# Kernel optimization log

Measured on AMD Instinct MI355X. Metric: run time of the kernel, lower is better.

## Reference

```python
import jax, jax.numpy as jnp
import numpy as np

B = 64                      # batch_size
MAX_STEPS = 100
FEAT = 6 + MAX_STEPS        # 106
REPEATS = 10
D = REPEATS * FEAT          # 1060
H = 256                     # policy_hidden_size
COUNTS = 32 * np.arange(B) + 16   # ragged segment sizes, sum=65536, max=2032
N = int(COUNTS.sum())
MAXLEN = int(COUNTS.max())
BN_EPS = 1e-5
LRELU_SLOPE = 0.01


def setup_inputs() -> dict:
    key = jax.random.key(0)
    k = jax.random.split(key, 6)
    seg = np.repeat(np.arange(B), COUNTS).astype(np.float32)  # column 0 = batch index
    features = jax.random.normal(k[0], (N, 1 + FEAT), jnp.float32)
    features = features.at[:, 0].set(jnp.asarray(seg))
    W1 = jax.random.normal(k[1], (D, H), jnp.float32) / np.sqrt(D)
    b1 = jax.random.normal(k[2], (H,), jnp.float32) * 0.01
    W2 = jax.random.normal(k[3], (H, 1), jnp.float32) / np.sqrt(H)
    b2 = jax.random.normal(k[4], (1,), jnp.float32) * 0.01
    return {
        "features": features,
        "bn_gamma": jnp.ones((D,), jnp.float32),
        "bn_beta": jnp.zeros((D,), jnp.float32),
        "W1": W1, "b1": b1, "W2": W2, "b2": b2,
        "max_len": MAXLEN,
    }


def reference(features, bn_gamma, bn_beta, W1, b1, W2, b2, max_len):
    seg = features[:, 0].astype(jnp.int32)                 # [N] batch indices
    x = jnp.tile(features[:, 1:], (1, REPEATS))            # [N, D] repeated features
    # BatchNorm1d (training mode: biased batch stats, as in the torch default)
    mean = jnp.mean(x, axis=0)
    var = jnp.var(x, axis=0)
    xn = (x - mean) * jax.lax.rsqrt(var + BN_EPS) * bn_gamma + bn_beta
    h = jnp.dot(xn, W1) + b1                               # [N, H]
    h = jnp.where(h >= 0, h, LRELU_SLOPE * h)              # LeakyReLU
    logits = (jnp.dot(h, W2) + b2)[:, 0]                   # [N]
    # segmented (ragged) log_softmax over each batch element's nodes
    m = jax.ops.segment_max(logits, seg, num_segments=B)   # [B]
    z = logits - m[seg]
    s = jax.ops.segment_sum(jnp.exp(z), seg, num_segments=B)
    logp = z - jnp.log(s)[seg]                             # [N]
    # scatter into padded [B, max_len] (-inf padding), position = rank within segment
    cnts = jax.ops.segment_sum(jnp.ones_like(seg), seg, num_segments=B)
    starts = jnp.cumsum(cnts) - cnts                       # exclusive prefix sum
    pos = jnp.arange(N, dtype=jnp.int32) - starts[seg]
    out = jnp.full((B, max_len), -jnp.inf, jnp.float32)
    return out.at[seg, pos].set(logp)
```

## Files before the change

kernel.cpp:

```cpp
#include <hip/hip_runtime.h>
#include <math.h>

#define NROWS   65536
#define NFEAT   106
#define NCOLIN  107
#define DREP    10
#define HID     256
#define BATCH   64
#define MAXLEN  2032
#define BN_EPS  1e-5f
#define SLOPE   0.01f
#define KPAD    128
#define NB_STATS 512
#define NEG_BIG (-1.0e30f)

#define WS_PART   0
#define WS_BACC   (WS_PART + NB_STATS*212)
#define WS_W1T    (WS_BACC + HID)
#define WS_FT     (WS_W1T + (HID*KPAD)/2)
#define WS_LOGITS (WS_FT + (NROWS*KPAD)/2)

typedef __attribute__((ext_vector_type(8))) short short8v;
typedef __attribute__((ext_vector_type(4))) float f32x4;

__device__ inline unsigned short f2bf(float x) {
    unsigned int u = __float_as_uint(x);
    return (unsigned short)((u + 0x7FFFu + ((u >> 16) & 1u)) >> 16);
}

__device__ __forceinline__ void gload_lds16(const void* g, void* l) {
    __builtin_amdgcn_global_load_lds(
        (const __attribute__((address_space(1))) void*)(g),
        (__attribute__((address_space(3))) void*)(l), 16, 0, 0);
}

__global__ __launch_bounds__(256) void k_stats(const float* __restrict__ feat,
                                               const float* __restrict__ b1,
                                               float* __restrict__ ws) {
    int tid  = threadIdx.x;
    int wave = tid >> 6, lane = tid & 63;
    int gw   = blockIdx.x * 4 + wave;
    if (blockIdx.x == 0) ws[WS_BACC + tid] = b1[tid];

    unsigned char* ft = (unsigned char*)(ws + WS_FT);
    int c0 = 2 * lane, c1 = 2 * lane + 1;
    bool act = (lane < 53);
    float s0 = 0.f, q0 = 0.f, s1 = 0.f, q1 = 0.f;
    for (int r = gw; r < NROWS; r += 2048) {
        const float* row = feat + (size_t)r * NCOLIN + 1;
        float v0 = 0.f, v1 = 0.f;
        if (act) { v0 = row[c0]; v1 = row[c1]; }
        s0 += v0; q0 += v0 * v0;
        s1 += v1; q1 += v1 * v1;
        unsigned int u = ((unsigned int)f2bf(v1) << 16) | f2bf(v0);
        *(unsigned int*)(ft + (size_t)r * 256 + lane * 4) = u;
    }
    __shared__ float red[4][64][4];
    red[wave][lane][0] = s0; red[wave][lane][1] = q0;
    red[wave][lane][2] = s1; red[wave][lane][3] = q1;
    __syncthreads();
    if (tid < 53) {
        float S0 = 0.f, Q0 = 0.f, S1 = 0.f, Q1 = 0.f;
        for (int w = 0; w < 4; ++w) {
            S0 += red[w][tid][0]; Q0 += red[w][tid][1];
            S1 += red[w][tid][2]; Q1 += red[w][tid][3];
        }
        float* p = ws + WS_PART + blockIdx.x * 212;
        p[2 * tid] = S0; p[2 * tid + 1] = S1;
        p[106 + 2 * tid] = Q0; p[107 + 2 * tid] = Q1;
    }
}

__global__ __launch_bounds__(256) void k_fold2(const float* __restrict__ gamma,
                                               const float* __restrict__ beta,
                                               const float* __restrict__ W1,
                                               float* __restrict__ ws) {
    int k = blockIdx.x;
    int j = threadIdx.x;
    unsigned char* w1t = (unsigned char*)(ws + WS_W1T);
    int byteW = j * 256 + ((2 * k) ^ ((j & 7) << 4));
    if (k >= NFEAT) { *(unsigned short*)(w1t + byteW) = 0; return; }

    float S = ws[WS_PART + j * 212 + k]       + ws[WS_PART + (j + 256) * 212 + k];
    float Q = ws[WS_PART + j * 212 + 106 + k] + ws[WS_PART + (j + 256) * 212 + 106 + k];
    #pragma unroll
    for (int o = 32; o > 0; o >>= 1) { S += __shfl_xor(S, o); Q += __shfl_xor(Q, o); }
    __shared__ float r8[8];
    int w = j >> 6, l = j & 63;
    if (l == 0) { r8[w * 2] = S; r8[w * 2 + 1] = Q; }
    __syncthreads();
    S = r8[0] + r8[2] + r8[4] + r8[6];
    Q = r8[1] + r8[3] + r8[5] + r8[7];

    float mean = S * (1.0f / NROWS);
    float var  = Q * (1.0f / NROWS) - mean * mean;
    float rstd = rsqrtf(var + BN_EPS);

    float accW = 0.f, accB = 0.f;
    #pragma unroll
    for (int r = 0; r < DREP; ++r) {
        int d = r * NFEAT + k;
        float wv = W1[(size_t)d * HID + j];
        accW += gamma[d] * wv;
        accB += beta[d]  * wv;
    }
    float a = accW * rstd;
    *(unsigned short*)(w1t + byteW) = f2bf(a);
    atomicAdd(&ws[WS_BACC + j], accB - mean * a);
}

__global__ __launch_bounds__(256) void k_mlp4(const float* __restrict__ W2,
                                              const float* __restrict__ b2,
                                              float* __restrict__ ws) {
    __shared__ __align__(16) unsigned char wl[65536];
    int tid = threadIdx.x;
    int w = tid >> 6, l = tid & 63;
    int lq = l >> 4, ln = l & 15;

    const unsigned char* wsrc = (const unsigned char*)(ws + WS_W1T);
    #pragma unroll
    for (int i = 0; i < 16; ++i)
        gload_lds16(wsrc + (w * 16 + i) * 1024 + l * 16, wl + (w * 16 + i) * 1024);

    int rowBase = blockIdx.x * 128 + w * 32;
    const unsigned char* ab = (const unsigned char*)(ws + WS_FT) + (size_t)rowBase * 256;
    short8v a[2][4];
    #pragma unroll
    for (int t = 0; t < 2; ++t)
        #pragma unroll
        for (int ks = 0; ks < 4; ++ks)
            a[t][ks] = *(const short8v*)(ab + t * 4096 + ln * 256 + ks * 64 + lq * 16);

    float b1r[16], w2r[16];
    #pragma unroll
    for (int ct = 0; ct < 16; ++ct) {
        b1r[ct] = ws[WS_BACC + ct * 16 + ln];
        w2r[ct] = W2[ct * 16 + ln];
    }
    float bias2 = b2[0];
    __syncthreads();

    float sp[2][4] = {{0.f,0.f,0.f,0.f},{0.f,0.f,0.f,0.f}};
    #pragma unroll
    for (int ct = 0; ct < 16; ++ct) {
        int j = ct * 16 + ln;
        int sw = (j & 7) << 4;
        short8v bq[4];
        #pragma unroll
        for (int ks = 0; ks < 4; ++ks)
            bq[ks] = *(const short8v*)(wl + j * 256 + ((ks * 64 + lq * 16) ^ sw));
        #pragma unroll
        for (int t = 0; t < 2; ++t) {
            f32x4 acc = {b1r[ct], b1r[ct], b1r[ct], b1r[ct]};
            #pragma unroll
            for (int ks = 0; ks < 4; ++ks)
                acc = __builtin_amdgcn_mfma_f32_16x16x32_bf16(a[t][ks], bq[ks], acc, 0, 0, 0);
            #pragma unroll
            for (int reg = 0; reg < 4; ++reg) {
                float h = acc[reg];
                h = (h >= 0.f) ? h : SLOPE * h;
                sp[t][reg] += h * w2r[ct];
            }
        }
    }
    #pragma unroll
    for (int t = 0; t < 2; ++t)
        #pragma unroll
        for (int reg = 0; reg < 4; ++reg) {
            float s = sp[t][reg];
            s += __shfl_xor(s, 1); s += __shfl_xor(s, 2);
            s += __shfl_xor(s, 4); s += __shfl_xor(s, 8);
            if (ln == 0)
                ws[WS_LOGITS + rowBase + t * 16 + lq * 4 + reg] = s + bias2;
        }
}

__global__ __launch_bounds__(256) void k_softmax(const float* __restrict__ ws,
                                                 float* __restrict__ out) {
    int b = blockIdx.x;
    int tid = threadIdx.x;
    int cnt = 32 * b + 16;
    int start = 16 * b * b;
    __shared__ float cache[MAXLEN];
    __shared__ float red[8];
    const float* lg = ws + WS_LOGITS + start;
    for (int i = tid; i < cnt; i += 256) cache[i] = lg[i];
    __syncthreads();

    float m = -1.0e30f;
    for (int i = tid; i < cnt; i += 256) m = fmaxf(m, cache[i]);
    #pragma unroll
    for (int o = 32; o > 0; o >>= 1) m = fmaxf(m, __shfl_xor(m, o));
    int wave = tid >> 6, lane = tid & 63;
    if (lane == 0) red[wave] = m;
    __syncthreads();
    m = fmaxf(fmaxf(red[0], red[1]), fmaxf(red[2], red[3]));

    float s = 0.f;
    for (int i = tid; i < cnt; i += 256) s += expf(cache[i] - m);
    #pragma unroll
    for (int o = 32; o > 0; o >>= 1) s += __shfl_xor(s, o);
    if (lane == 0) red[4 + wave] = s;
    __syncthreads();
    s = red[4] + red[5] + red[6] + red[7];
    float logC = m + logf(s);

    float* op = out + (size_t)b * MAXLEN;
    for (int i = tid; i < MAXLEN; i += 256)
        op[i] = (i < cnt) ? cache[i] - logC : NEG_BIG;
}

extern "C" void kernel_launch(void* const* d_in, const int* in_sizes, int n_in,
                              void* d_out, int out_size, void* d_ws, size_t ws_size,
                              hipStream_t stream) {
    const float* feat  = (const float*)d_in[0];
    const float* gamma = (const float*)d_in[1];
    const float* beta  = (const float*)d_in[2];
    const float* W1    = (const float*)d_in[3];
    const float* b1    = (const float*)d_in[4];
    const float* W2    = (const float*)d_in[5];
    const float* b2    = (const float*)d_in[6];
    float* ws  = (float*)d_ws;
    float* out = (float*)d_out;

    hipLaunchKernelGGL(k_stats,   dim3(NB_STATS), dim3(256), 0, stream, feat, b1, ws);
    hipLaunchKernelGGL(k_fold2,   dim3(KPAD),     dim3(256), 0, stream, gamma, beta, W1, ws);
    hipLaunchKernelGGL(k_mlp4,    dim3(512),      dim3(256), 0, stream, W2, b2, ws);
    hipLaunchKernelGGL(k_softmax, dim3(BATCH),    dim3(256), 0, stream, ws, out);
}
```

Before: 40.62 us.

## Fuse MLP logits with segmented softmax in one per-segment kernel

Merges the MLP and softmax kernels so each block computes the logits of one batch segment straight into shared memory and then runs the log-softmax. This removes one launch and the global logits round trip, and adds register prefetch of the next weight tile. The cost is a grid of only 64 blocks with uneven work, so the largest segment sets the time and most compute units sit idle. The stats kernel also switches to contiguous row chunks per wave.

```diff
diff --git a/kernel.cpp b/kernel.cpp
--- a/kernel.cpp
+++ b/kernel.cpp
@@ -18,7 +18,6 @@
 #define WS_BACC   (WS_PART + NB_STATS*212)
 #define WS_W1T    (WS_BACC + HID)
 #define WS_FT     (WS_W1T + (HID*KPAD)/2)
-#define WS_LOGITS (WS_FT + (NROWS*KPAD)/2)
 
 typedef __attribute__((ext_vector_type(8))) short short8v;
 typedef __attribute__((ext_vector_type(4))) float f32x4;
@@ -39,14 +38,16 @@
                                                float* __restrict__ ws) {
     int tid  = threadIdx.x;
     int wave = tid >> 6, lane = tid & 63;
-    int gw   = blockIdx.x * 4 + wave;
     if (blockIdx.x == 0) ws[WS_BACC + tid] = b1[tid];
 
     unsigned char* ft = (unsigned char*)(ws + WS_FT);
-    int c0 = 2 * lane, c1 = 2 * lane + 1;
+    int c0 = 2 * lane, c1 = c0 + 1;
     bool act = (lane < 53);
+    int r0 = blockIdx.x * 128 + wave * 32;
     float s0 = 0.f, q0 = 0.f, s1 = 0.f, q1 = 0.f;
-    for (int r = gw; r < NROWS; r += 2048) {
+    #pragma unroll 4
+    for (int i = 0; i < 32; ++i) {
+        int r = r0 + i;
         const float* row = feat + (size_t)r * NCOLIN + 1;
         float v0 = 0.f, v1 = 0.f;
         if (act) { v0 = row[c0]; v1 = row[c1]; }
@@ -109,27 +110,25 @@
     atomicAdd(&ws[WS_BACC + j], accB - mean * a);
 }
 
-__global__ __launch_bounds__(256) void k_mlp4(const float* __restrict__ W2,
-                                              const float* __restrict__ b2,
-                                              float* __restrict__ ws) {
+__global__ __launch_bounds__(256) void k_mlpsm(const float* __restrict__ W2,
+                                               const float* __restrict__ b2,
+                                               float* __restrict__ ws,
+                                               float* __restrict__ out) {
     __shared__ __align__(16) unsigned char wl[65536];
+    __shared__ float cache[MAXLEN];
+    __shared__ float red[8];
     int tid = threadIdx.x;
     int w = tid >> 6, l = tid & 63;
     int lq = l >> 4, ln = l & 15;
+    int b = blockIdx.x;
+    int cnt = 32 * b + 16;
+    int start = 16 * b * b;
+    int ntiles = cnt >> 4;
 
     const unsigned char* wsrc = (const unsigned char*)(ws + WS_W1T);
     #pragma unroll
     for (int i = 0; i < 16; ++i)
         gload_lds16(wsrc + (w * 16 + i) * 1024 + l * 16, wl + (w * 16 + i) * 1024);
-
-    int rowBase = blockIdx.x * 128 + w * 32;
-    const unsigned char* ab = (const unsigned char*)(ws + WS_FT) + (size_t)rowBase * 256;
-    short8v a[2][4];
-    #pragma unroll
-    for (int t = 0; t < 2; ++t)
-        #pragma unroll
-        for (int ks = 0; ks < 4; ++ks)
-            a[t][ks] = *(const short8v*)(ab + t * 4096 + ln * 256 + ks * 64 + lq * 16);
 
     float b1r[16], w2r[16];
     #pragma unroll
@@ -140,59 +139,70 @@
     float bias2 = b2[0];
     __syncthreads();
 
-    float sp[2][4] = {{0.f,0.f,0.f,0.f},{0.f,0.f,0.f,0.f}};
-    #pragma unroll
-    for (int ct = 0; ct < 16; ++ct) {
-        int j = ct * 16 + ln;
-        int sw = (j & 7) << 4;
-        short8v bq[4];
-        #pragma unroll
-        for (int ks = 0; ks < 4; ++ks)
-            bq[ks] = *(const short8v*)(wl + j * 256 + ((ks * 64 + lq * 16) ^ sw));
-        #pragma unroll
-        for (int t = 0; t < 2; ++t) {
-            f32x4 acc = {b1r[ct], b1r[ct], b1r[ct], b1r[ct]};
+    const unsigned char* ab = (const unsigned char*)(ws + WS_FT) + (size_t)start * 256;
+    int sw = (ln & 7) << 4;
+
+    for (int t0 = 4 * w; t0 < ntiles; t0 += 16) {
+        short8v a[4][4];
+        #pragma unroll
+        for (int u = 0; u < 4; ++u) {
+            int t = t0 + u;
+            int tc = (t < ntiles) ? t : t0;
+            const unsigned char* ap = ab + (size_t)tc * 4096 + ln * 256 + lq * 16;
             #pragma unroll
             for (int ks = 0; ks < 4; ++ks)
-                acc = __builtin_amdgcn_mfma_f32_16x16x32_bf16(a[t][ks], bq[ks], acc, 0, 0, 0);
+                a[u][ks] = *(const short8v*)(ap + ks * 64);
+        }
+        float sp[4][4] = {{0,0,0,0},{0,0,0,0},{0,0,0,0},{0,0,0,0}};
+        short8v bqc[4], bqn[4];
+        #pragma unroll
+        for (int ks = 0; ks < 4; ++ks)
+            bqc[ks] = *(const short8v*)(wl + ln * 256 + ((ks * 64 + lq * 16) ^ sw));
+        #pragma unroll
+        for (int ct = 0; ct < 16; ++ct) {
+            if (ct < 15) {
+                int j = (ct + 1) * 16 + ln;
+                #pragma unroll
+                for (int ks = 0; ks < 4; ++ks)
+                    bqn[ks] = *(const short8v*)(wl + j * 256 + ((ks * 64 + lq * 16) ^ sw));
+            }
             #pragma unroll
-            for (int reg = 0; reg < 4; ++reg) {
-                float h = acc[reg];
-                h = (h >= 0.f) ? h : SLOPE * h;
-                sp[t][reg] += h * w2r[ct];
+            for (int u = 0; u < 4; ++u) {
+                f32x4 acc = {b1r[ct], b1r[ct], b1r[ct], b1r[ct]};
+                #pragma unroll
+                for (int ks = 0; ks < 4; ++ks)
+                    acc = __builtin_amdgcn_mfma_f32_16x16x32_bf16(a[u][ks], bqc[ks], acc, 0, 0, 0);
+                #pragma unroll
+                for (int reg = 0; reg < 4; ++reg) {
+                    float h = acc[reg];
+                    h = (h >= 0.f) ? h : SLOPE * h;
+                    sp[u][reg] += h * w2r[ct];
+                }
             }
-        }
-    }
-    #pragma unroll
-    for (int t = 0; t < 2; ++t)
-        #pragma unroll
-        for (int reg = 0; reg < 4; ++reg) {
-            float s = sp[t][reg];
-            s += __shfl_xor(s, 1); s += __shfl_xor(s, 2);
-            s += __shfl_xor(s, 4); s += __shfl_xor(s, 8);
-            if (ln == 0)
-                ws[WS_LOGITS + rowBase + t * 16 + lq * 4 + reg] = s + bias2;
-        }
-}
-
-__global__ __launch_bounds__(256) void k_softmax(const float* __restrict__ ws,
-                                                 float* __restrict__ out) {
-    int b = blockIdx.x;
-    int tid = threadIdx.x;
-    int cnt = 32 * b + 16;
-    int start = 16 * b * b;
-    __shared__ float cache[MAXLEN];
-    __shared__ float red[8];
-    const float* lg = ws + WS_LOGITS + start;
-    for (int i = tid; i < cnt; i += 256) cache[i] = lg[i];
+            #pragma unroll
+            for (int ks = 0; ks < 4; ++ks) bqc[ks] = bqn[ks];
+        }
+        #pragma unroll
+        for (int u = 0; u < 4; ++u) {
+            int t = t0 + u;
+            if (t < ntiles) {
+                #pragma unroll
+                for (int reg = 0; reg < 4; ++reg) {
+                    float s = sp[u][reg];
+                    s += __shfl_xor(s, 1); s += __shfl_xor(s, 2);
+                    s += __shfl_xor(s, 4); s += __shfl_xor(s, 8);
+                    if (ln == 0) cache[t * 16 + lq * 4 + reg] = s + bias2;
+                }
+            }
+        }
+    }
     __syncthreads();
 
     float m = -1.0e30f;
     for (int i = tid; i < cnt; i += 256) m = fmaxf(m, cache[i]);
     #pragma unroll
     for (int o = 32; o > 0; o >>= 1) m = fmaxf(m, __shfl_xor(m, o));
-    int wave = tid >> 6, lane = tid & 63;
-    if (lane == 0) red[wave] = m;
+    if (l == 0) red[w] = m;
     __syncthreads();
     m = fmaxf(fmaxf(red[0], red[1]), fmaxf(red[2], red[3]));
 
@@ -200,7 +210,7 @@
     for (int i = tid; i < cnt; i += 256) s += expf(cache[i] - m);
     #pragma unroll
     for (int o = 32; o > 0; o >>= 1) s += __shfl_xor(s, o);
-    if (lane == 0) red[4 + wave] = s;
+    if (l == 0) red[4 + w] = s;
     __syncthreads();
     s = red[4] + red[5] + red[6] + red[7];
     float logC = m + logf(s);
@@ -223,8 +233,7 @@
     float* ws  = (float*)d_ws;
     float* out = (float*)d_out;
 
-    hipLaunchKernelGGL(k_stats,   dim3(NB_STATS), dim3(256), 0, stream, feat, b1, ws);
-    hipLaunchKernelGGL(k_fold2,   dim3(KPAD),     dim3(256), 0, stream, gamma, beta, W1, ws);
-    hipLaunchKernelGGL(k_mlp4,    dim3(512),      dim3(256), 0, stream, W2, b2, ws);
-    hipLaunchKernelGGL(k_softmax, dim3(BATCH),    dim3(256), 0, stream, ws, out);
-}
+    hipLaunchKernelGGL(k_stats, dim3(NB_STATS), dim3(256), 0, stream, feat, b1, ws);
+    hipLaunchKernelGGL(k_fold2, dim3(KPAD),     dim3(256), 0, stream, gamma, beta, W1, ws);
+    hipLaunchKernelGGL(k_mlpsm, dim3(BATCH),    dim3(256), 0, stream, W2, b2, ws, out);
+}
```

Result: slower. 129.6 us (+219.0%).

## Fuse segmented softmax into MLP kernel via last-block-done counters

Applied to the files above, without the earlier changes.

Removes the separate softmax launch. Each MLP block atomically adds its row contributions to per-segment counters, and the block that completes a segment runs that segment's log-softmax and writes the padded output row. The stats kernel also switches to contiguous 32-row chunks per wave, and LeakyReLU becomes an fmax. This saves a launch and its dependency gap, but the softmax tail is serialized onto whichever block finishes each segment and relies on threadfence ordering between blocks.

```diff
diff --git a/kernel.cpp b/kernel.cpp
--- a/kernel.cpp
+++ b/kernel.cpp
@@ -19,6 +19,7 @@
 #define WS_W1T    (WS_BACC + HID)
 #define WS_FT     (WS_W1T + (HID*KPAD)/2)
 #define WS_LOGITS (WS_FT + (NROWS*KPAD)/2)
+#define WS_CTR    (WS_LOGITS + NROWS)
 
 typedef __attribute__((ext_vector_type(8))) short short8v;
 typedef __attribute__((ext_vector_type(4))) float f32x4;
@@ -39,14 +40,16 @@
                                                float* __restrict__ ws) {
     int tid  = threadIdx.x;
     int wave = tid >> 6, lane = tid & 63;
-    int gw   = blockIdx.x * 4 + wave;
     if (blockIdx.x == 0) ws[WS_BACC + tid] = b1[tid];
 
     unsigned char* ft = (unsigned char*)(ws + WS_FT);
-    int c0 = 2 * lane, c1 = 2 * lane + 1;
+    int c0 = 2 * lane, c1 = c0 + 1;
     bool act = (lane < 53);
+    int r0 = blockIdx.x * 128 + wave * 32;
     float s0 = 0.f, q0 = 0.f, s1 = 0.f, q1 = 0.f;
-    for (int r = gw; r < NROWS; r += 2048) {
+    #pragma unroll 4
+    for (int i = 0; i < 32; ++i) {
+        int r = r0 + i;
         const float* row = feat + (size_t)r * NCOLIN + 1;
         float v0 = 0.f, v1 = 0.f;
         if (act) { v0 = row[c0]; v1 = row[c1]; }
@@ -77,6 +80,7 @@
                                                float* __restrict__ ws) {
     int k = blockIdx.x;
     int j = threadIdx.x;
+    if (j == 0 && k < BATCH) ((int*)(ws + WS_CTR))[k] = 0;
     unsigned char* w1t = (unsigned char*)(ws + WS_W1T);
     int byteW = j * 256 + ((2 * k) ^ ((j & 7) << 4));
     if (k >= NFEAT) { *(unsigned short*)(w1t + byteW) = 0; return; }
@@ -109,10 +113,15 @@
     atomicAdd(&ws[WS_BACC + j], accB - mean * a);
 }
 
-__global__ __launch_bounds__(256) void k_mlp4(const float* __restrict__ W2,
+__global__ __launch_bounds__(256) void k_mlp5(const float* __restrict__ W2,
                                               const float* __restrict__ b2,
-                                              float* __restrict__ ws) {
+                                              float* __restrict__ ws,
+                                              float* __restrict__ out) {
     __shared__ __align__(16) unsigned char wl[65536];
+    __shared__ float cache[MAXLEN];
+    __shared__ float red[8];
+    __shared__ int wins[4];
+    __shared__ int nwin;
     int tid = threadIdx.x;
     int w = tid >> 6, l = tid & 63;
     int lq = l >> 4, ln = l & 15;
@@ -158,7 +167,7 @@
             #pragma unroll
             for (int reg = 0; reg < 4; ++reg) {
                 float h = acc[reg];
-                h = (h >= 0.f) ? h : SLOPE * h;
+                h = fmaxf(h, SLOPE * h);
                 sp[t][reg] += h * w2r[ct];
             }
         }
@@ -173,41 +182,60 @@
             if (ln == 0)
                 ws[WS_LOGITS + rowBase + t * 16 + lq * 4 + reg] = s + bias2;
         }
-}
-
-__global__ __launch_bounds__(256) void k_softmax(const float* __restrict__ ws,
-                                                 float* __restrict__ out) {
-    int b = blockIdx.x;
-    int tid = threadIdx.x;
-    int cnt = 32 * b + 16;
-    int start = 16 * b * b;
-    __shared__ float cache[MAXLEN];
-    __shared__ float red[8];
-    const float* lg = ws + WS_LOGITS + start;
-    for (int i = tid; i < cnt; i += 256) cache[i] = lg[i];
-    __syncthreads();
-
-    float m = -1.0e30f;
-    for (int i = tid; i < cnt; i += 256) m = fmaxf(m, cache[i]);
-    #pragma unroll
-    for (int o = 32; o > 0; o >>= 1) m = fmaxf(m, __shfl_xor(m, o));
-    int wave = tid >> 6, lane = tid & 63;
-    if (lane == 0) red[wave] = m;
-    __syncthreads();
-    m = fmaxf(fmaxf(red[0], red[1]), fmaxf(red[2], red[3]));
-
-    float s = 0.f;
-    for (int i = tid; i < cnt; i += 256) s += expf(cache[i] - m);
-    #pragma unroll
-    for (int o = 32; o > 0; o >>= 1) s += __shfl_xor(s, o);
-    if (lane == 0) red[4 + wave] = s;
-    __syncthreads();
-    s = red[4] + red[5] + red[6] + red[7];
-    float logC = m + logf(s);
-
-    float* op = out + (size_t)b * MAXLEN;
-    for (int i = tid; i < MAXLEN; i += 256)
-        op[i] = (i < cnt) ? cache[i] - logC : NEG_BIG;
+    __syncthreads();
+
+    if (tid == 0) {
+        nwin = 0;
+        __threadfence();
+        int R0 = blockIdx.x * 128, R1 = R0 + 128;
+        int s = (int)sqrtf((float)R0 * 0.0625f);
+        while (s > 0 && 16 * s * s > R0) --s;
+        while (16 * (s + 1) * (s + 1) <= R0) ++s;
+        int* ctr = (int*)(ws + WS_CTR);
+        while (s < BATCH && 16 * s * s < R1) {
+            int lo = 16 * s * s;       if (lo < R0) lo = R0;
+            int hi = 16 * (s+1)*(s+1); if (hi > R1) hi = R1;
+            int contrib = hi - lo;
+            int old = atomicAdd(&ctr[s], contrib);
+            if (old + contrib == 32 * s + 16) wins[nwin++] = s;
+            ++s;
+        }
+    }
+    __syncthreads();
+    int nw = nwin;
+    if (nw == 0) return;
+    __threadfence();
+
+    for (int iw = 0; iw < nw; ++iw) {
+        int sseg = wins[iw];
+        int cnt = 32 * sseg + 16;
+        int start = 16 * sseg * sseg;
+        const float* lg = ws + WS_LOGITS + start;
+        for (int i = tid; i < cnt; i += 256) cache[i] = lg[i];
+        __syncthreads();
+
+        float m = -1.0e30f;
+        for (int i = tid; i < cnt; i += 256) m = fmaxf(m, cache[i]);
+        #pragma unroll
+        for (int o = 32; o > 0; o >>= 1) m = fmaxf(m, __shfl_xor(m, o));
+        if (l == 0) red[w] = m;
+        __syncthreads();
+        m = fmaxf(fmaxf(red[0], red[1]), fmaxf(red[2], red[3]));
+
+        float s = 0.f;
+        for (int i = tid; i < cnt; i += 256) s += expf(cache[i] - m);
+        #pragma unroll
+        for (int o = 32; o > 0; o >>= 1) s += __shfl_xor(s, o);
+        if (l == 0) red[4 + w] = s;
+        __syncthreads();
+        s = red[4] + red[5] + red[6] + red[7];
+        float logC = m + logf(s);
+
+        float* op = out + (size_t)sseg * MAXLEN;
+        for (int i = tid; i < MAXLEN; i += 256)
+            op[i] = (i < cnt) ? cache[i] - logC : NEG_BIG;
+        __syncthreads();
+    }
 }
 
 extern "C" void kernel_launch(void* const* d_in, const int* in_sizes, int n_in,
@@ -223,8 +251,7 @@
     float* ws  = (float*)d_ws;
     float* out = (float*)d_out;
 
-    hipLaunchKernelGGL(k_stats,   dim3(NB_STATS), dim3(256), 0, stream, feat, b1, ws);
-    hipLaunchKernelGGL(k_fold2,   dim3(KPAD),     dim3(256), 0, stream, gamma, beta, W1, ws);
-    hipLaunchKernelGGL(k_mlp4,    dim3(512),      dim3(256), 0, stream, W2, b2, ws);
-    hipLaunchKernelGGL(k_softmax, dim3(BATCH),    dim3(256), 0, stream, ws, out);
-}
+    hipLaunchKernelGGL(k_stats, dim3(NB_STATS), dim3(256), 0, stream, feat, b1, ws);
+    hipLaunchKernelGGL(k_fold2, dim3(KPAD),     dim3(256), 0, stream, gamma, beta, W1, ws);
+    hipLaunchKernelGGL(k_mlp5,  dim3(512),      dim3(256), 0, stream, W2, b2, ws, out);
+}
```

After: 60.69 us. 1.49x slower.
